# Optimization experiments

Hardware: AMD Instinct MI355X
Metric: run time of the kernel (lower is better)

## Reference

```python
import jax, jax.numpy as jnp
import numpy as np

NB = 50  # nb_steps
IN_D = 64
HID = 128
B = 256


def _cc_weights(nb):
    # Faithful port of UMNN compute_cc_weights (Clenshaw-Curtis quadrature)
    lam = np.arange(0, nb + 1).reshape(-1, 1).astype(np.float64)
    lam = np.cos((lam @ lam.T) * np.pi / nb)
    lam[:, 0] = 0.5
    lam[:, -1] = 0.5 * lam[:, -1]
    lam = lam * 2.0 / nb
    W = np.arange(0, nb + 1).reshape(-1, 1).astype(np.float64)
    W[np.arange(1, nb + 1, 2)] = 0
    W = 2.0 / (1.0 - W ** 2)
    W[0] = 1
    W[np.arange(1, nb + 1, 2)] = 0
    cc = (lam.T @ W)[:, 0].astype(np.float32)              # [nb+1]
    steps = np.cos(np.arange(0, nb + 1) * np.pi / nb).astype(np.float32)  # [nb+1]
    return jnp.asarray(cc), jnp.asarray(steps)


def setup_inputs() -> dict:
    key = jax.random.key(0)
    ks = jax.random.split(key, 16)
    d = {}
    d["x"] = jax.random.normal(ks[0], (B, 1), dtype=jnp.float32)
    d["h"] = jax.random.normal(ks[1], (B, IN_D - 1), dtype=jnp.float32)

    def lin(kw, kb, fan_in, fan_out):
        s = 1.0 / np.sqrt(fan_in)
        w = jax.random.uniform(kw, (fan_in, fan_out), jnp.float32, -s, s)
        b = jax.random.uniform(kb, (fan_out,), jnp.float32, -s, s)
        return w, b

    # Integrand MLP: in_d -> 128 -> 128 -> 1
    d["iw0"], d["ib0"] = lin(ks[2], ks[3], IN_D, HID)
    d["iw1"], d["ib1"] = lin(ks[4], ks[5], HID, HID)
    d["iw2"], d["ib2"] = lin(ks[6], ks[7], HID, 1)
    # Outer net: (in_d-1) -> 128 -> 128 -> 2
    d["nw0"], d["nb0"] = lin(ks[8], ks[9], IN_D - 1, HID)
    d["nw1"], d["nb1"] = lin(ks[10], ks[11], HID, HID)
    d["nw2"], d["nb2"] = lin(ks[12], ks[13], HID, 2)
    return d


def reference(x, h, iw0, ib0, iw1, ib1, iw2, ib2, nw0, nb0, nw1, nb1, nw2, nb2):
    cc, steps = _cc_weights(NB)  # [S1], [S1]
    S1 = NB + 1
    b = x.shape[0]

    # ----- outer quadrature: integral over t in [0, x] -----
    # t[b, i] = 0 + (x - 0) * (steps[i] + 1) / 2
    t = x[:, None, :] * (steps[None, :, None] + 1.0) / 2.0          # [B, S1, 1]

    # ----- inner UMNN: integral over s in [t, xmax], xmax = max(t) + 10 -----
    xmax = jnp.max(t) + 10.0
    s = t[:, :, None, :] + (xmax - t)[:, :, None, :] * (steps[None, None, :, None] + 1.0) / 2.0  # [B,S1,S1,1]

    hb = jnp.broadcast_to(h[:, None, None, :], (b, S1, S1, h.shape[1]))
    inp = jnp.concatenate([s, hb], axis=-1)                         # [B,S1,S1,in_d]

    # PostiveIntegrandNN: Lin-ReLU-Lin-ReLU-Lin-ELU, then + 1.0
    a = jax.nn.relu(inp @ iw0 + ib0)
    a = jax.nn.relu(a @ iw1 + ib1)
    f = jax.nn.elu(a @ iw2 + ib2) + 1.0                              # [B,S1,S1,1]

    # inner Clenshaw-Curtis reduction: z * (xT - x0) / 2
    inner = jnp.sum(f * cc[None, None, :, None], axis=2) * (xmax - t) / 2.0   # [B,S1,1]

    # outer reduction: integral from 0 to x
    outer = jnp.sum(inner * cc[None, :, None], axis=1) * x / 2.0    # [B,1]

    # outer dense net on h -> offset / scaling
    o = jax.nn.relu(h @ nw0 + nb0)
    o = jax.nn.relu(o @ nw1 + nb1)
    o = o @ nw2 + nb2                                               # [B,2]
    offset = o[:, 0:1]
    scaling = jnp.exp(o[:, 1:2])
    return scaling * outer + offset
```

## Files before the change

### kernel.cpp

```cpp
#include <hip/hip_runtime.h>
#include <math.h>

#define NBQ 50
#define S1 51
#define NPTS 2601
#define NTILES 163
#define IN_D 64
#define HID 128
#define BSZ 256
#define NCHUNK 8

typedef __bf16 bf16x8 __attribute__((ext_vector_type(8)));
typedef float  f32x4  __attribute__((ext_vector_type(4)));

#define WS_CC     0
#define WS_STEPS  64
#define WS_XMAX   128
#define WS_BASE   256
#define WS_SCAL   33024
#define WS_OFF    33280
#define WS_PART   33536
#define WS_W1BF   35840

__global__ void k_prep(const float* __restrict__ x, const float* __restrict__ h,
                       const float* __restrict__ iw0, const float* __restrict__ ib0,
                       const float* __restrict__ iw1,
                       const float* __restrict__ nw0, const float* __restrict__ nb0,
                       const float* __restrict__ nw1, const float* __restrict__ nb1,
                       const float* __restrict__ nw2, const float* __restrict__ nb2,
                       float* __restrict__ ws) {
    int blk = blockIdx.x;
    int tid = threadIdx.x;

    if (blk < 64) {
        int idx  = blk * 256 + tid;
        int e    = idx & 7;
        int lane = (idx >> 3) & 63;
        int fk   = idx >> 9;
        int kk   = fk & 3;
        int nt   = fk >> 2;
        int k = kk * 32 + (lane >> 4) * 8 + e;
        int n = nt * 16 + (lane & 15);
        __bf16* w1bf = (__bf16*)(ws + WS_W1BF);
        w1bf[idx] = (__bf16)iw1[k * HID + n];
        return;
    }

    __shared__ float s_steps[S1];
    __shared__ float s_red[4];
    __shared__ float s_h[IN_D - 1];
    __shared__ float s_o0[HID];
    __shared__ float s_part[4];

    if (blk == 64) {
        int t = tid;
        if (t < S1) {
            double st = cos((double)t * M_PI / (double)NBQ);
            s_steps[t] = (float)st;
            ws[WS_STEPS + t] = (float)st;
            double acc = 0.0;
            for (int i = 0; i <= NBQ; ++i) {
                double Wi;
                if (i == 0)       Wi = 1.0;
                else if (i & 1)   Wi = 0.0;
                else              Wi = 2.0 / (1.0 - (double)i * (double)i);
                double lam;
                if (t == 0)  lam = 0.5;
                else         lam = cos((double)i * (double)t * M_PI / (double)NBQ);
                if (t == NBQ) lam *= 0.5;
                lam *= 2.0 / (double)NBQ;
                acc += lam * Wi;
            }
            ws[WS_CC + t] = (float)acc;
        }
        __syncthreads();
        float xb = x[t];
        float m = -1e30f;
        for (int i = 0; i < S1; ++i)
            m = fmaxf(m, xb * (s_steps[i] + 1.0f) * 0.5f);
        for (int off = 32; off > 0; off >>= 1)
            m = fmaxf(m, __shfl_down(m, off));
        if ((t & 63) == 0) s_red[t >> 6] = m;
        __syncthreads();
        if (t == 0) {
            float mm = fmaxf(fmaxf(s_red[0], s_red[1]), fmaxf(s_red[2], s_red[3]));
            ws[WS_XMAX] = mm + 10.0f;
        }
        return;
    }

    int b = blk - 65;
    int n = tid;
    bool act = (n < HID);
    if (act && n < IN_D - 1) s_h[n] = h[b * (IN_D - 1) + n];
    __syncthreads();
    float o1 = 0.0f;
    if (act) {
        float accB = ib0[n];
        float acc0 = nb0[n];
        for (int d = 0; d < IN_D - 1; ++d) {
            float hv = s_h[d];
            accB = fmaf(hv, iw0[(1 + d) * HID + n], accB);
            acc0 = fmaf(hv, nw0[d * HID + n], acc0);
        }
        ws[WS_BASE + b * HID + n] = accB;
        s_o0[n] = fmaxf(acc0, 0.0f);
    }
    __syncthreads();
    if (act) {
        float acc1 = nb1[n];
        for (int m = 0; m < HID; ++m)
            acc1 = fmaf(s_o0[m], nw1[m * HID + n], acc1);
        o1 = fmaxf(acc1, 0.0f);
    }
    float p0 = act ? o1 * nw2[n * 2 + 0] : 0.0f;
    float p1 = act ? o1 * nw2[n * 2 + 1] : 0.0f;
    for (int off = 32; off > 0; off >>= 1) {
        p0 += __shfl_down(p0, off);
        p1 += __shfl_down(p1, off);
    }
    int lane = tid & 63, w = tid >> 6;
    if (lane == 0 && w < 2) { s_part[w * 2] = p0; s_part[w * 2 + 1] = p1; }
    __syncthreads();
    if (tid == 0) {
        ws[WS_OFF + b]  = s_part[0] + s_part[2] + nb2[0];
        ws[WS_SCAL + b] = expf(s_part[1] + s_part[3] + nb2[1]);
    }
}

__global__ __launch_bounds__(128, 2) void k3_mfma(
        const float* __restrict__ x,
        const float* __restrict__ iw0,
        const float* __restrict__ ib1,
        const float* __restrict__ iw2,
        const float* __restrict__ ib2,
        float* __restrict__ ws) {
    __shared__ float s_cc[S1];
    __shared__ float s_ti[S1];
    __shared__ float s_w[S1];
    __shared__ float s_sjh[S1];
    __shared__ float s_ccw[S1];
    __shared__ float s_z[2][16];

    int blk  = blockIdx.x;
    int b    = blk >> 3;
    int c    = blk & 7;
    int tid  = threadIdx.x;
    int wave = tid >> 6;
    int lane = tid & 63;
    int col  = lane & 15;
    int g    = lane >> 4;

    float xmax = ws[WS_XMAX];
    float xb   = x[b];
    float b2   = ib2[0];

    if (tid < S1) {
        float st = ws[WS_STEPS + tid];
        float cc = ws[WS_CC + tid];
        float ti = xb * (st + 1.0f) * 0.5f;
        float w  = xmax - ti;
        s_cc[tid]  = cc;
        s_ti[tid]  = ti;
        s_w[tid]   = w;
        s_sjh[tid] = (st + 1.0f) * 0.5f;
        s_ccw[tid] = cc * w;
    }

    const bf16x8* w1f = (const bf16x8*)(ws + WS_W1BF);
    bf16x8 Af[4][4];
#pragma unroll
    for (int nt = 0; nt < 4; ++nt) {
        int NT = wave * 4 + nt;
#pragma unroll
        for (int kk = 0; kk < 4; ++kk)
            Af[nt][kk] = w1f[(NT * 4 + kk) * 64 + lane];
    }

    const float* basep = ws + WS_BASE + b * HID;
    f32x4 w0a[4], w0b[4], bsa[4], bsb[4];
#pragma unroll
    for (int kk = 0; kk < 4; ++kk) {
        int m0 = kk * 32 + g * 8;
        w0a[kk] = *(const f32x4*)(iw0 + m0);
        w0b[kk] = *(const f32x4*)(iw0 + m0 + 4);
        bsa[kk] = *(const f32x4*)(basep + m0);
        bsb[kk] = *(const f32x4*)(basep + m0 + 4);
    }

    f32x4 accInit[4], iw2v[4];
#pragma unroll
    for (int nt = 0; nt < 4; ++nt) {
        int n0 = (wave * 4 + nt) * 16 + g * 4;
        accInit[nt] = *(const f32x4*)(ib1 + n0);
        iw2v[nt]    = *(const f32x4*)(iw2 + n0);
    }

    __syncthreads();

    float vsum = 0.0f;
    int par = 0;

    for (int t = c; t < NTILES; t += NCHUNK) {
        int p  = t * 16 + col;
        int pc = (p < NPTS) ? p : (NPTS - 1);
        int i  = (int)(((unsigned)pc * 10281u) >> 19);
        int j  = pc - i * 51;
        float s = fmaf(s_w[i], s_sjh[j], s_ti[i]);

        f32x4 acc[4];
#pragma unroll
        for (int kk = 0; kk < 4; ++kk) {
            bf16x8 bfr;
#pragma unroll
            for (int e = 0; e < 4; ++e) {
                bfr[e]     = (__bf16)fmaxf(fmaf(s, w0a[kk][e], bsa[kk][e]), 0.0f);
                bfr[4 + e] = (__bf16)fmaxf(fmaf(s, w0b[kk][e], bsb[kk][e]), 0.0f);
            }
#pragma unroll
            for (int nt = 0; nt < 4; ++nt)
                acc[nt] = __builtin_amdgcn_mfma_f32_16x16x32_bf16(
                    Af[nt][kk], bfr, (kk == 0) ? accInit[nt] : acc[nt], 0, 0, 0);
        }

        float z = 0.0f;
#pragma unroll
        for (int nt = 0; nt < 4; ++nt)
#pragma unroll
            for (int q = 0; q < 4; ++q)
                z = fmaf(fmaxf(acc[nt][q], 0.0f), iw2v[nt][q], z);
        z += __shfl_xor(z, 16);
        z += __shfl_xor(z, 32);

        if (wave == 0 && g == 0) s_z[par][col] = z;
        __syncthreads();
        if (wave == 1) {
            float zf = z + s_z[par][col] + b2;
            float f  = (zf > 0.0f) ? (zf + 1.0f) : __expf(zf);
            float val = s_ccw[i] * s_cc[j] * f;
            vsum += (p < NPTS) ? val : 0.0f;
        }
        par ^= 1;
    }

    if (wave == 1) {
#pragma unroll
        for (int off = 1; off < 64; off <<= 1)
            vsum += __shfl_xor(vsum, off);
        if (lane == 0)
            ws[WS_PART + blk] = vsum * 0.125f;
    }
}

__global__ void k4_final(const float* __restrict__ x, const float* __restrict__ ws,
                         float* __restrict__ out) {
    int b = threadIdx.x;
    float sum = 0.0f;
#pragma unroll
    for (int c = 0; c < NCHUNK; ++c) sum += ws[WS_PART + b * NCHUNK + c];
    out[b] = ws[WS_SCAL + b] * sum * x[b] * 0.5f + ws[WS_OFF + b];
}

extern "C" void kernel_launch(void* const* d_in, const int* in_sizes, int n_in,
                              void* d_out, int out_size, void* d_ws, size_t ws_size,
                              hipStream_t stream) {
    const float* x   = (const float*)d_in[0];
    const float* h   = (const float*)d_in[1];
    const float* iw0 = (const float*)d_in[2];
    const float* ib0 = (const float*)d_in[3];
    const float* iw1 = (const float*)d_in[4];
    const float* ib1 = (const float*)d_in[5];
    const float* iw2 = (const float*)d_in[6];
    const float* ib2 = (const float*)d_in[7];
    const float* nw0 = (const float*)d_in[8];
    const float* nb0 = (const float*)d_in[9];
    const float* nw1 = (const float*)d_in[10];
    const float* nb1 = (const float*)d_in[11];
    const float* nw2 = (const float*)d_in[12];
    const float* nb2 = (const float*)d_in[13];
    float* ws  = (float*)d_ws;
    float* out = (float*)d_out;

    hipLaunchKernelGGL(k_prep, dim3(64 + 1 + BSZ), dim3(256), 0, stream,
                       x, h, iw0, ib0, iw1, nw0, nb0, nw1, nb1, nw2, nb2, ws);
    hipLaunchKernelGGL(k3_mfma, dim3(BSZ * NCHUNK), dim3(128), 0, stream,
                       x, iw0, ib1, iw2, ib2, ws);
    hipLaunchKernelGGL(k4_final, dim3(1), dim3(BSZ), 0, stream, x, ws, out);
}
```

Before: 57.49 us.

## Split integrand MLP across four waves with LDS-shared double-buffered activations

The MFMA kernel now uses 256 threads (four waves) per block instead of two. Each wave computes one 32-wide K-slice of the first-layer bf16 activations, stores it in double-buffered LDS, and then runs two 16-column N tiles using all four slices. Per-wave partial outputs are staged in LDS and reduced in a final pass, which also stops the old kernel counting every point four times in its reduction. The goal is to cut per-thread register load (fewer A fragments and first-layer weights) so occupancy and latency hiding improve, at the cost of more LDS traffic and block barriers.

After: 50.42 us. -12.3%, faster.

```diff
diff --git a/kernel.cpp b/kernel.cpp
--- a/kernel.cpp
+++ b/kernel.cpp
@@ -9,6 +9,7 @@
 #define HID 128
 #define BSZ 256
 #define NCHUNK 8
+#define NUMAX 21
 
 typedef __bf16 bf16x8 __attribute__((ext_vector_type(8)));
 typedef float  f32x4  __attribute__((ext_vector_type(4)));
@@ -20,7 +21,7 @@
 #define WS_SCAL   33024
 #define WS_OFF    33280
 #define WS_PART   33536
-#define WS_W1BF   35840
+#define WS_W1BF   41728
 
 __global__ void k_prep(const float* __restrict__ x, const float* __restrict__ h,
                        const float* __restrict__ iw0, const float* __restrict__ ib0,
@@ -128,7 +129,7 @@
     }
 }
 
-__global__ __launch_bounds__(128, 2) void k3_mfma(
+__global__ __launch_bounds__(256, 3) void k3_mfma(
         const float* __restrict__ x,
         const float* __restrict__ iw0,
         const float* __restrict__ ib1,
@@ -140,7 +141,8 @@
     __shared__ float s_w[S1];
     __shared__ float s_sjh[S1];
     __shared__ float s_ccw[S1];
-    __shared__ float s_z[2][16];
+    __shared__ bf16x8 bfr_lds[2][4][4][64];
+    __shared__ float zlds[4][NUMAX][17];
 
     int blk  = blockIdx.x;
     int b    = blk >> 3;
@@ -168,88 +170,134 @@
     }
 
     const bf16x8* w1f = (const bf16x8*)(ws + WS_W1BF);
-    bf16x8 Af[4][4];
-#pragma unroll
-    for (int nt = 0; nt < 4; ++nt) {
-        int NT = wave * 4 + nt;
+    bf16x8 Af[2][4];
+#pragma unroll
+    for (int nt = 0; nt < 2; ++nt) {
+        int NT = wave * 2 + nt;
 #pragma unroll
         for (int kk = 0; kk < 4; ++kk)
             Af[nt][kk] = w1f[(NT * 4 + kk) * 64 + lane];
     }
 
     const float* basep = ws + WS_BASE + b * HID;
-    f32x4 w0a[4], w0b[4], bsa[4], bsb[4];
-#pragma unroll
-    for (int kk = 0; kk < 4; ++kk) {
-        int m0 = kk * 32 + g * 8;
-        w0a[kk] = *(const f32x4*)(iw0 + m0);
-        w0b[kk] = *(const f32x4*)(iw0 + m0 + 4);
-        bsa[kk] = *(const f32x4*)(basep + m0);
-        bsb[kk] = *(const f32x4*)(basep + m0 + 4);
-    }
-
-    f32x4 accInit[4], iw2v[4];
-#pragma unroll
-    for (int nt = 0; nt < 4; ++nt) {
-        int n0 = (wave * 4 + nt) * 16 + g * 4;
+    int m0 = wave * 32 + g * 8;
+    f32x4 w0a = *(const f32x4*)(iw0 + m0);
+    f32x4 w0b = *(const f32x4*)(iw0 + m0 + 4);
+    f32x4 bsa = *(const f32x4*)(basep + m0);
+    f32x4 bsb = *(const f32x4*)(basep + m0 + 4);
+
+    f32x4 accInit[2], iw2v[2];
+#pragma unroll
+    for (int nt = 0; nt < 2; ++nt) {
+        int n0 = (wave * 2 + nt) * 16 + g * 4;
         accInit[nt] = *(const f32x4*)(ib1 + n0);
         iw2v[nt]    = *(const f32x4*)(iw2 + n0);
     }
 
-    __syncthreads();
+    int NU = (c <= 2) ? 21 : 20;
+    int G  = (NU + 3) >> 2;
+
+    __syncthreads();
+
+#pragma unroll
+    for (int t = 0; t < 4; ++t) {
+        int u = t;
+        if (u < NU) {
+            int p  = (c + 8 * u) * 16 + col;
+            int pc = (p < NPTS) ? p : (NPTS - 1);
+            int i  = (int)(((unsigned)pc * 10281u) >> 19);
+            int j  = pc - i * 51;
+            float s = fmaf(s_w[i], s_sjh[j], s_ti[i]);
+            bf16x8 bfr;
+#pragma unroll
+            for (int e = 0; e < 4; ++e) {
+                bfr[e]     = (__bf16)fmaxf(fmaf(s, w0a[e], bsa[e]), 0.0f);
+                bfr[4 + e] = (__bf16)fmaxf(fmaf(s, w0b[e], bsb[e]), 0.0f);
+            }
+            bfr_lds[0][t][wave][lane] = bfr;
+        }
+    }
+    __syncthreads();
+
+    for (int grp = 0; grp < G; ++grp) {
+        int nb = grp + 1;
+        if (nb < G) {
+            int ubase = nb * 4;
+#pragma unroll
+            for (int t = 0; t < 4; ++t) {
+                int u = ubase + t;
+                if (u < NU) {
+                    int p  = (c + 8 * u) * 16 + col;
+                    int pc = (p < NPTS) ? p : (NPTS - 1);
+                    int i  = (int)(((unsigned)pc * 10281u) >> 19);
+                    int j  = pc - i * 51;
+                    float s = fmaf(s_w[i], s_sjh[j], s_ti[i]);
+                    bf16x8 bfr;
+#pragma unroll
+                    for (int e = 0; e < 4; ++e) {
+                        bfr[e]     = (__bf16)fmaxf(fmaf(s, w0a[e], bsa[e]), 0.0f);
+                        bfr[4 + e] = (__bf16)fmaxf(fmaf(s, w0b[e], bsb[e]), 0.0f);
+                    }
+                    bfr_lds[nb & 1][t][wave][lane] = bfr;
+                }
+            }
+        }
+
+        int buf = grp & 1;
+        int ubase = grp * 4;
+#pragma unroll
+        for (int t = 0; t < 4; ++t) {
+            int u = ubase + t;
+            if (u < NU) {
+                bf16x8 f0 = bfr_lds[buf][t][0][lane];
+                bf16x8 f1 = bfr_lds[buf][t][1][lane];
+                bf16x8 f2 = bfr_lds[buf][t][2][lane];
+                bf16x8 f3 = bfr_lds[buf][t][3][lane];
+                f32x4 a0 = __builtin_amdgcn_mfma_f32_16x16x32_bf16(Af[0][0], f0, accInit[0], 0, 0, 0);
+                f32x4 a1 = __builtin_amdgcn_mfma_f32_16x16x32_bf16(Af[1][0], f0, accInit[1], 0, 0, 0);
+                a0 = __builtin_amdgcn_mfma_f32_16x16x32_bf16(Af[0][1], f1, a0, 0, 0, 0);
+                a1 = __builtin_amdgcn_mfma_f32_16x16x32_bf16(Af[1][1], f1, a1, 0, 0, 0);
+                a0 = __builtin_amdgcn_mfma_f32_16x16x32_bf16(Af[0][2], f2, a0, 0, 0, 0);
+                a1 = __builtin_amdgcn_mfma_f32_16x16x32_bf16(Af[1][2], f2, a1, 0, 0, 0);
+                a0 = __builtin_amdgcn_mfma_f32_16x16x32_bf16(Af[0][3], f3, a0, 0, 0, 0);
+                a1 = __builtin_amdgcn_mfma_f32_16x16x32_bf16(Af[1][3], f3, a1, 0, 0, 0);
+
+                float za = 0.f, zb = 0.f;
+#pragma unroll
+                for (int q = 0; q < 4; ++q) {
+                    za = fmaf(fmaxf(a0[q], 0.0f), iw2v[0][q], za);
+                    zb = fmaf(fmaxf(a1[q], 0.0f), iw2v[1][q], zb);
+                }
+                float z = za + zb;
+                z += __shfl_xor(z, 16);
+                z += __shfl_xor(z, 32);
+                if (lane < 16) zlds[wave][u][lane] = z;
+            }
+        }
+        __syncthreads();
+    }
 
     float vsum = 0.0f;
-    int par = 0;
-
-    for (int t = c; t < NTILES; t += NCHUNK) {
-        int p  = t * 16 + col;
-        int pc = (p < NPTS) ? p : (NPTS - 1);
-        int i  = (int)(((unsigned)pc * 10281u) >> 19);
-        int j  = pc - i * 51;
-        float s = fmaf(s_w[i], s_sjh[j], s_ti[i]);
-
-        f32x4 acc[4];
-#pragma unroll
-        for (int kk = 0; kk < 4; ++kk) {
-            bf16x8 bfr;
-#pragma unroll
-            for (int e = 0; e < 4; ++e) {
-                bfr[e]     = (__bf16)fmaxf(fmaf(s, w0a[kk][e], bsa[kk][e]), 0.0f);
-                bfr[4 + e] = (__bf16)fmaxf(fmaf(s, w0b[kk][e], bsb[kk][e]), 0.0f);
-            }
-#pragma unroll
-            for (int nt = 0; nt < 4; ++nt)
-                acc[nt] = __builtin_amdgcn_mfma_f32_16x16x32_bf16(
-                    Af[nt][kk], bfr, (kk == 0) ? accInit[nt] : acc[nt], 0, 0, 0);
-        }
-
-        float z = 0.0f;
-#pragma unroll
-        for (int nt = 0; nt < 4; ++nt)
-#pragma unroll
-            for (int q = 0; q < 4; ++q)
-                z = fmaf(fmaxf(acc[nt][q], 0.0f), iw2v[nt][q], z);
-        z += __shfl_xor(z, 16);
-        z += __shfl_xor(z, 32);
-
-        if (wave == 0 && g == 0) s_z[par][col] = z;
-        __syncthreads();
-        if (wave == 1) {
-            float zf = z + s_z[par][col] + b2;
-            float f  = (zf > 0.0f) ? (zf + 1.0f) : __expf(zf);
-            float val = s_ccw[i] * s_cc[j] * f;
-            vsum += (p < NPTS) ? val : 0.0f;
-        }
-        par ^= 1;
-    }
-
-    if (wave == 1) {
-#pragma unroll
-        for (int off = 1; off < 64; off <<= 1)
-            vsum += __shfl_xor(vsum, off);
-        if (lane == 0)
-            ws[WS_PART + blk] = vsum * 0.125f;
-    }
+    int npass = (NU + 15) >> 4;
+    for (int pass = 0; pass < npass; ++pass) {
+        int u = pass * 16 + wave * 4 + g;
+        if (u < NU) {
+            int p = (c + 8 * u) * 16 + col;
+            if (p < NPTS) {
+                float z = zlds[0][u][col] + zlds[1][u][col]
+                        + zlds[2][u][col] + zlds[3][u][col] + b2;
+                float f = (z > 0.0f) ? (z + 1.0f) : __expf(z);
+                int i = (int)(((unsigned)p * 10281u) >> 19);
+                int j = p - i * 51;
+                vsum += s_ccw[i] * s_cc[j] * f;
+            }
+        }
+    }
+#pragma unroll
+    for (int off = 1; off < 64; off <<= 1)
+        vsum += __shfl_xor(vsum, off);
+    if (lane == 0)
+        ws[WS_PART + blk * 4 + wave] = vsum * 0.5f;
 }
 
 __global__ void k4_final(const float* __restrict__ x, const float* __restrict__ ws,
@@ -257,7 +305,7 @@
     int b = threadIdx.x;
     float sum = 0.0f;
 #pragma unroll
-    for (int c = 0; c < NCHUNK; ++c) sum += ws[WS_PART + b * NCHUNK + c];
+    for (int c = 0; c < 32; ++c) sum += ws[WS_PART + b * 32 + c];
     out[b] = ws[WS_SCAL + b] * sum * x[b] * 0.5f + ws[WS_OFF + b];
 }
 
@@ -283,7 +331,7 @@
 
     hipLaunchKernelGGL(k_prep, dim3(64 + 1 + BSZ), dim3(256), 0, stream,
                        x, h, iw0, ib0, iw1, nw0, nb0, nw1, nb1, nw2, nb2, ws);
-    hipLaunchKernelGGL(k3_mfma, dim3(BSZ * NCHUNK), dim3(128), 0, stream,
+    hipLaunchKernelGGL(k3_mfma, dim3(BSZ * NCHUNK), dim3(256), 0, stream,
                        x, iw0, ib1, iw2, ib2, ws);
     hipLaunchKernelGGL(k4_final, dim3(1), dim3(BSZ), 0, stream, x, ws, out);
 }
```
